# Performance work log

Measured on AMD Instinct MI355X. Metric: run time of the kernel, lower is better.

Reference implementation:

```python
import jax, jax.numpy as jnp
import numpy as np

EPS = 1e-5        # BatchNorm eps (torch default)
ALPHA = 0.2       # LeakyReLU negative slope


def _gather_nbrs(x, idx):
    # x: (B,N,C), idx: (B,P,S) -> (B,P,S,C)
    B, P, S = idx.shape
    flat = jnp.take_along_axis(x, idx.reshape(B, P * S, 1), axis=1)
    return flat.reshape(B, P, S, x.shape[-1])


def _mlp_layer(x, w, b, g, bt, m, v):
    # 1x1 Conv2d == channel matmul; BN in eval mode with running stats; ReLU.
    h = x @ w.T + b
    h = (h - m) * jax.lax.rsqrt(v + EPS) * g + bt
    return jax.nn.relu(h)


def setup_inputs() -> dict:
    key = jax.random.key(0)
    ks = jax.random.split(key, 8)
    B, N, P, S, C = 16, 4096, 1024, 32, 64
    inp = {
        "xyz": jax.random.normal(ks[0], (B, 3, N), dtype=jnp.float32),
        "points": jax.random.normal(ks[1], (B, C, N), dtype=jnp.float32),
        "fps_idx": jax.random.randint(ks[2], (B, P), 0, N, dtype=jnp.int32),
        "group_idx": jax.random.randint(ks[3], (B, P, S), 0, N, dtype=jnp.int32),
    }
    chans = [(64, 67), (64, 64), (128, 64)]
    for i, (co, ci) in enumerate(chans, start=1):
        kk = jax.random.fold_in(key, 100 + i)
        inp[f"w{i}"] = jax.random.normal(kk, (co, ci), dtype=jnp.float32) * (1.0 / np.sqrt(ci))
        inp[f"b{i}"] = jnp.zeros((co,), jnp.float32)
        inp[f"g{i}"] = jnp.ones((co,), jnp.float32)
        inp[f"beta{i}"] = jnp.zeros((co,), jnp.float32)
        inp[f"m{i}"] = jnp.zeros((co,), jnp.float32)
        inp[f"v{i}"] = jnp.ones((co,), jnp.float32)
    inp["a"] = jax.random.normal(ks[4], (3 + 128, 128), dtype=jnp.float32) * 0.1
    return inp


def reference(xyz, points, fps_idx, group_idx,
              w1, b1, g1, beta1, m1, v1,
              w2, b2, g2, beta2, m2, v2,
              w3, b3, g3, beta3, m3, v3, a):
    xyz_p = jnp.transpose(xyz, (0, 2, 1))      # (B,N,3)
    pts_p = jnp.transpose(points, (0, 2, 1))   # (B,N,C)

    # sample_and_group with precomputed fps / ball-query indices
    new_xyz = jnp.take_along_axis(xyz_p, fps_idx[:, :, None], axis=1)   # (B,P,3)
    fps_feat = jnp.take_along_axis(pts_p, fps_idx[:, :, None], axis=1)  # (B,P,C)
    grouped_xyz = _gather_nbrs(xyz_p, group_idx) - new_xyz[:, :, None, :]  # relative (B,P,S,3)
    grouped_feat = _gather_nbrs(pts_p, group_idx)                           # (B,P,S,C)

    new_points = jnp.concatenate([grouped_xyz, grouped_feat], axis=-1)  # (B,P,S,3+C)
    fps_points = jnp.concatenate([new_xyz, fps_feat], axis=-1)          # (B,P,3+C)

    layers = [(w1, b1, g1, beta1, m1, v1), (w2, b2, g2, beta2, m2, v2), (w3, b3, g3, beta3, m3, v3)]
    for (w, b, g, bt, m, v) in layers:
        new_points = _mlp_layer(new_points, w, b, g, bt, m, v)
        fps_points = _mlp_layer(fps_points, w, b, g, bt, m, v)

    # GraphAttention: delta features -> leaky-relu scores -> softmax over neighbors -> pool
    delta_p = new_xyz[:, :, None, :] - grouped_xyz        # (B,P,S,3)
    delta_h = fps_points[:, :, None, :] - new_points       # (B,P,S,D)
    e = jnp.concatenate([delta_p, delta_h], axis=-1) @ a   # (B,P,S,D)
    e = jnp.where(e > 0, e, ALPHA * e)
    attn = jax.nn.softmax(e, axis=2)                       # softmax over nsample
    pooled = jnp.sum(attn * new_points, axis=2)            # (B,P,D)

    return jnp.transpose(new_xyz, (0, 2, 1)), jnp.transpose(pooled, (0, 2, 1))
```

## Files before the change

kernel.cpp:

```cpp
#include <hip/hip_runtime.h>
#include <hip/hip_bf16.h>

#define Bn 16
#define Nn 4096
#define Pn 1024
#define Sn 32
#define Cn 64
#define EPSn 1e-5f
#define ALPHAn 0.2f

#define W1O 0
#define W2O 4352
#define W3O 8448
#define AO  16640
#define B1O 33536
#define B2O 33600
#define B3O 33664
#define WSF 33792
__device__ __align__(16) float g_W[WSF];

#define F1F 0
#define F2F 24
#define F3F 40
#define F5F 72
#define NFRAG 152
#define WFU (NFRAG * 512)
__device__ __align__(16) unsigned short g_Wf[WFU];

__device__ __align__(16) float g_pts[Bn * Nn * 68];
__device__ __align__(16) float g_fps[Bn * Pn * 132];
__device__ __align__(16) float g_tmp[Bn * Pn * 128];

typedef __attribute__((ext_vector_type(8))) short short8;
typedef __attribute__((ext_vector_type(4))) float f32x4;

__device__ __forceinline__ void split2(float v, unsigned short& hu, unsigned short& lu) {
  __hip_bfloat16 h = __float2bfloat16(v);
  float hv = __bfloat162float(h);
  __hip_bfloat16 l = __float2bfloat16(v - hv);
  hu = *(unsigned short*)&h;
  lu = *(unsigned short*)&l;
}
__device__ __forceinline__ unsigned short bfh(float v) {
  __hip_bfloat16 h = __float2bfloat16(v);
  return *(unsigned short*)&h;
}
__device__ __forceinline__ float bf2f(unsigned short u) {
  __hip_bfloat16 h = *(__hip_bfloat16*)&u;
  return __bfloat162float(h);
}

__global__ __launch_bounds__(256) void prep_kernel(
    const float* __restrict__ xyz, const float* __restrict__ points,
    const float* __restrict__ w1, const float* __restrict__ b1,
    const float* __restrict__ g1, const float* __restrict__ bt1,
    const float* __restrict__ m1, const float* __restrict__ v1,
    const float* __restrict__ w2, const float* __restrict__ b2,
    const float* __restrict__ g2, const float* __restrict__ bt2,
    const float* __restrict__ m2, const float* __restrict__ v2,
    const float* __restrict__ w3, const float* __restrict__ b3,
    const float* __restrict__ g3, const float* __restrict__ bt3,
    const float* __restrict__ m3, const float* __restrict__ v3,
    const float* __restrict__ a)
{
  if (blockIdx.x < 1024) {
    __shared__ float T[68 * 65];
    const int t = threadIdx.x;
    const int b = blockIdx.x >> 6, n0 = (blockIdx.x & 63) << 6;
    const int nn = t & 63, cgrp = t >> 6;
    #pragma unroll
    for (int k = 0; k < 16; ++k) {
      const int c = cgrp * 16 + k;
      T[c * 65 + nn] = points[(b * Cn + c) * Nn + n0 + nn];
    }
    if (cgrp == 0) {
      #pragma unroll
      for (int d = 0; d < 3; ++d)
        T[(64 + d) * 65 + nn] = xyz[(b * 3 + d) * Nn + n0 + nn];
      T[67 * 65 + nn] = 0.f;
    }
    __syncthreads();
    const int row = t >> 2, part = t & 3;
    float* dst = g_pts + (((long)b << 12) + n0 + row) * 68 + part * 16;
    #pragma unroll
    for (int j = 0; j < 4; ++j) {
      const int o = part * 16 + j * 4;
      float4 v = { T[(o + 0) * 65 + row], T[(o + 1) * 65 + row],
                   T[(o + 2) * 65 + row], T[(o + 3) * 65 + row] };
      *(float4*)(dst + j * 4) = v;
    }
    if (part == 3) {
      float4 v = { T[64 * 65 + row], T[65 * 65 + row],
                   T[66 * 65 + row], T[67 * 65 + row] };
      *(float4*)(dst + 16) = v;
    }
    return;
  }
  const int idx = (blockIdx.x - 1024) * blockDim.x + threadIdx.x;
  if (idx < WSF) {
    float val;
    if (idx < W2O) {
      const int k = idx >> 6, o = idx & 63;
      const float sc = g1[o] * rsqrtf(v1[o] + EPSn);
      val = (k < 64) ? w1[o * 67 + 3 + k] * sc
          : (k < 67) ? w1[o * 67 + (k - 64)] * sc : 0.f;
    } else if (idx < W3O) {
      const int r = idx - W2O, k = r >> 6, o = r & 63;
      val = w2[o * 64 + k] * (g2[o] * rsqrtf(v2[o] + EPSn));
    } else if (idx < AO) {
      const int r = idx - W3O, k = r >> 7, o = r & 127;
      val = w3[o * 64 + k] * (g3[o] * rsqrtf(v3[o] + EPSn));
    } else if (idx < B1O) {
      int r = idx - AO;
      const int half = r / 8448; r -= half * 8448;
      const int k = r >> 6, o = half * 64 + (r & 63);
      val = (k < 128) ? a[(3 + k) * 128 + o]
          : (k < 131) ? a[(k - 128) * 128 + o] : 0.f;
    } else if (idx < B2O) {
      const int o = idx - B1O;
      val = (b1[o] - m1[o]) * (g1[o] * rsqrtf(v1[o] + EPSn)) + bt1[o];
    } else if (idx < B3O) {
      const int o = idx - B2O;
      val = (b2[o] - m2[o]) * (g2[o] * rsqrtf(v2[o] + EPSn)) + bt2[o];
    } else {
      const int o = idx - B3O;
      val = (b3[o] - m3[o]) * (g3[o] * rsqrtf(v3[o] + EPSn)) + bt3[o];
    }
    g_W[idx] = val;
  } else if (idx < WSF + WFU) {
    const int i = idx - WSF;
    const int frag = i >> 9, r = i & 511;
    const int lane = r >> 3, j = r & 7;
    const int quad = lane >> 4, nn = lane & 15;
    int plane, n, k;
    float w;
    if (frag < F2F) {
      const int f = frag;
      plane = f & 1;
      const int c = (f >> 1) & 1, kcch = f >> 2, kc = kcch % 3, ch = kcch / 3;
      n = ch * 32 + c * 16 + nn; k = kc * 32 + quad * 8 + j;
      const float s = g1[n] * rsqrtf(v1[n] + EPSn);
      w = (k < 64) ? w1[n * 67 + 3 + k] * s
        : (k < 67) ? w1[n * 67 + (k - 64)] * s : 0.f;
    } else if (frag < F3F) {
      const int f = frag - F2F;
      plane = f & 1;
      const int c = (f >> 1) & 1, kc = (f >> 2) & 1, ch = f >> 3;
      n = ch * 32 + c * 16 + nn; k = kc * 32 + quad * 8 + j;
      w = w2[n * 64 + k] * (g2[n] * rsqrtf(v2[n] + EPSn));
    } else if (frag < F5F) {
      const int f = frag - F3F;
      plane = f & 1;
      const int c = (f >> 1) & 3, kc = (f >> 3) & 1, ch = f >> 4;
      n = ch * 64 + c * 16 + nn; k = kc * 32 + quad * 8 + j;
      w = w3[n * 64 + k] * (g3[n] * rsqrtf(v3[n] + EPSn));
    } else {
      const int f = frag - F5F;
      plane = f & 1;
      const int c = (f >> 1) & 3, kcch = f >> 3, kc = kcch % 5, ch = kcch / 5;
      n = ch * 64 + c * 16 + nn; k = kc * 32 + quad * 8 + j;
      w = (k < 128) ? a[(3 + k) * 128 + n]
        : (k < 131) ? a[(k - 128) * 128 + n] : 0.f;
    }
    unsigned short hu, lu; split2(w, hu, lu);
    g_Wf[i] = plane ? lu : hu;
  }
}

#define XAs 88
#define XHs 152

__global__ __launch_bounds__(256) void fps_kernel(
    const int* __restrict__ fps_idx, float* __restrict__ out)
{
  __shared__ __align__(16) unsigned char LB[30736];
  unsigned short* XAh = (unsigned short*)(LB + 0);
  unsigned short* XAl = (unsigned short*)(LB + 5632);
  unsigned short* XHh = (unsigned short*)(LB + 11264);
  unsigned short* XHl = (unsigned short*)(LB + 20992);
  unsigned short* ZS  = (unsigned short*)(LB + 30720);

  const int t = threadIdx.x, lane = t & 63, w = t >> 6;
  const int quad = lane >> 4, nn = lane & 15;
  const int ch = w >> 1, cl = w & 1;
  const int blk = ((blockIdx.x & 7) << 6) | (blockIdx.x >> 3);
  const int g0 = blk * 32;

  if (t < 4) ((float*)ZS)[t] = 0.f;

  {
    const int s0 = t >> 3, cg = t & 7;
    const int gp = g0 + s0, b = gp >> 10, p = gp & 1023;
    const int fi = fps_idx[gp];
    const float* frow = g_pts + (((long)b << 12) + fi) * 68;
    const int c0 = cg * 8;
    const float4 va = *(const float4*)(frow + c0);
    const float4 vb = *(const float4*)(frow + c0 + 4);
    short8 hv, lv;
    unsigned short hu, lu;
    split2(va.x, hu, lu); hv[0] = (short)hu; lv[0] = (short)lu;
    split2(va.y, hu, lu); hv[1] = (short)hu; lv[1] = (short)lu;
    split2(va.z, hu, lu); hv[2] = (short)hu; lv[2] = (short)lu;
    split2(va.w, hu, lu); hv[3] = (short)hu; lv[3] = (short)lu;
    split2(vb.x, hu, lu); hv[4] = (short)hu; lv[4] = (short)lu;
    split2(vb.y, hu, lu); hv[5] = (short)hu; lv[5] = (short)lu;
    split2(vb.z, hu, lu); hv[6] = (short)hu; lv[6] = (short)lu;
    split2(vb.w, hu, lu); hv[7] = (short)hu; lv[7] = (short)lu;
    *(short8*)(XAh + s0 * XAs + c0) = hv;
    *(short8*)(XAl + s0 * XAs + c0) = lv;
    if (cg == 0) {
      #pragma unroll
      for (int d = 0; d < 3; ++d) {
        const float v = frow[64 + d];
        unsigned short h2, l2; split2(v, h2, l2);
        XAh[s0 * XAs + 64 + d] = h2; XAl[s0 * XAs + 64 + d] = l2;
        XHh[s0 * XHs + 128 + d] = h2; XHl[s0 * XHs + 128 + d] = l2;
        out[(b * 3 + d) * Pn + p] = v;
        g_fps[(long)gp * 132 + 128 + d] = v;
      }
    } else if (cg == 1) {
      #pragma unroll
      for (int j = 0; j < 13; ++j) { XAh[s0 * XAs + 67 + j] = 0; XAl[s0 * XAs + 67 + j] = 0; }
    } else if (cg == 2) {
      #pragma unroll
      for (int j = 0; j < 13; ++j) { XHh[s0 * XHs + 131 + j] = 0; XHl[s0 * XHs + 131 + j] = 0; }
    }
  }
  __syncthreads();

#define MFMA_BF16 __builtin_amdgcn_mfma_f32_16x16x32_bf16
#define TERM3(Ci, Ahh, All, Bh, Bl) \
    Ci = MFMA_BF16(Ahh, Bh, Ci, 0, 0, 0); \
    Ci = MFMA_BF16(Ahh, Bl, Ci, 0, 0, 0); \
    Ci = MFMA_BF16(All, Bh, Ci, 0, 0, 0);

  f32x4 C[4];
  const int col1 = w * 16 + nn;

  C[0] = (f32x4){0.f,0.f,0.f,0.f}; C[1] = C[0];
  #pragma unroll
  for (int kc = 0; kc < 3; ++kc) {
    const int ka = kc * 32 + quad * 8;
    const short8 A0h = (ka < 80) ? *(const short8*)(XAh + nn * XAs + ka) : *(const short8*)ZS;
    const short8 A0l = (ka < 80) ? *(const short8*)(XAl + nn * XAs + ka) : *(const short8*)ZS;
    const short8 A1h = (ka < 80) ? *(const short8*)(XAh + (16 + nn) * XAs + ka) : *(const short8*)ZS;
    const short8 A1l = (ka < 80) ? *(const short8*)(XAl + (16 + nn) * XAs + ka) : *(const short8*)ZS;
    const unsigned short* pf = g_Wf + (((ch * 3 + kc) * 2 + cl) * 2) * 512 + lane * 8;
    const short8 Bh = *(const short8*)pf, Bl = *(const short8*)(pf + 512);
    TERM3(C[0], A0h, A0l, Bh, Bl);
    TERM3(C[1], A1h, A1l, Bh, Bl);
  }
  #pragma unroll
  for (int mi = 0; mi < 2; ++mi)
    #pragma unroll
    for (int r = 0; r < 4; ++r) {
      const float v = fmaxf(C[mi][r] + g_W[B1O + col1], 0.f);
      unsigned short hu, lu; split2(v, hu, lu);
      XHh[(mi * 16 + quad * 4 + r) * XHs + col1] = hu;
      XHl[(mi * 16 + quad * 4 + r) * XHs + col1] = lu;
    }
  __syncthreads();

  C[0] = (f32x4){0.f,0.f,0.f,0.f}; C[1] = C[0];
  #pragma unroll
  for (int kc = 0; kc < 2; ++kc) {
    const int ka = kc * 32 + quad * 8;
    const short8 A0h = *(const short8*)(XHh + nn * XHs + ka);
    const short8 A0l = *(const short8*)(XHl + nn * XHs + ka);
    const short8 A1h = *(const short8*)(XHh + (16 + nn) * XHs + ka);
    const short8 A1l = *(const short8*)(XHl + (16 + nn) * XHs + ka);
    const unsigned short* pf = g_Wf + (F2F + ((ch * 2 + kc) * 2 + cl) * 2) * 512 + lane * 8;
    const short8 Bh = *(const short8*)pf, Bl = *(const short8*)(pf + 512);
    TERM3(C[0], A0h, A0l, Bh, Bl);
    TERM3(C[1], A1h, A1l, Bh, Bl);
  }
  __syncthreads();
  #pragma unroll
  for (int mi = 0; mi < 2; ++mi)
    #pragma unroll
    for (int r = 0; r < 4; ++r) {
      const float v = fmaxf(C[mi][r] + g_W[B2O + col1], 0.f);
      unsigned short hu, lu; split2(v, hu, lu);
      XAh[(mi * 16 + quad * 4 + r) * XAs + col1] = hu;
      XAl[(mi * 16 + quad * 4 + r) * XAs + col1] = lu;
    }
  __syncthreads();

  #pragma unroll
  for (int i = 0; i < 4; ++i) C[i] = (f32x4){0.f,0.f,0.f,0.f};
  #pragma unroll
  for (int kc = 0; kc < 2; ++kc) {
    const int ka = kc * 32 + quad * 8;
    const short8 A0h = *(const short8*)(XAh + nn * XAs + ka);
    const short8 A0l = *(const short8*)(XAl + nn * XAs + ka);
    const short8 A1h = *(const short8*)(XAh + (16 + nn) * XAs + ka);
    const short8 A1l = *(const short8*)(XAl + (16 + nn) * XAs + ka);
    #pragma unroll
    for (int c2 = 0; c2 < 2; ++c2) {
      const unsigned short* pf = g_Wf + (F3F + ((ch * 2 + kc) * 4 + cl * 2 + c2) * 2) * 512 + lane * 8;
      const short8 Bh = *(const short8*)pf, Bl = *(const short8*)(pf + 512);
      TERM3(C[0 + c2], A0h, A0l, Bh, Bl);
      TERM3(C[2 + c2], A1h, A1l, Bh, Bl);
    }
  }
  __syncthreads();
  #pragma unroll
  for (int c2 = 0; c2 < 2; ++c2) {
    const int col = w * 32 + c2 * 16 + nn;
    #pragma unroll
    for (int mi = 0; mi < 2; ++mi)
      #pragma unroll
      for (int r = 0; r < 4; ++r) {
        const float v = fmaxf(C[mi * 2 + c2][r] + g_W[B3O + col], 0.f);
        unsigned short hu, lu; split2(v, hu, lu);
        XHh[(mi * 16 + quad * 4 + r) * XHs + col] = hu;
        XHl[(mi * 16 + quad * 4 + r) * XHs + col] = lu;
      }
  }
  __syncthreads();

  #pragma unroll
  for (int i = 0; i < 4; ++i) C[i] = (f32x4){0.f,0.f,0.f,0.f};
  #pragma unroll
  for (int kc = 0; kc < 5; ++kc) {
    const int ka = kc * 32 + quad * 8;
    const short8 A0h = (ka < 144) ? *(const short8*)(XHh + nn * XHs + ka) : *(const short8*)ZS;
    const short8 A0l = (ka < 144) ? *(const short8*)(XHl + nn * XHs + ka) : *(const short8*)ZS;
    const short8 A1h = (ka < 144) ? *(const short8*)(XHh + (16 + nn) * XHs + ka) : *(const short8*)ZS;
    const short8 A1l = (ka < 144) ? *(const short8*)(XHl + (16 + nn) * XHs + ka) : *(const short8*)ZS;
    #pragma unroll
    for (int c2 = 0; c2 < 2; ++c2) {
      const unsigned short* pf = g_Wf + (F5F + ((ch * 5 + kc) * 4 + cl * 2 + c2) * 2) * 512 + lane * 8;
      const short8 Bh = *(const short8*)pf, Bl = *(const short8*)(pf + 512);
      TERM3(C[0 + c2], A0h, A0l, Bh, Bl);
      TERM3(C[2 + c2], A1h, A1l, Bh, Bl);
    }
  }
  #pragma unroll
  for (int c2 = 0; c2 < 2; ++c2) {
    const int col = w * 32 + c2 * 16 + nn;
    #pragma unroll
    for (int mi = 0; mi < 2; ++mi)
      #pragma unroll
      for (int r = 0; r < 4; ++r)
        g_fps[(long)(g0 + mi * 16 + quad * 4 + r) * 132 + col] = C[mi * 2 + c2][r];
  }
}

__global__ __launch_bounds__(256) void transpose_out(float* __restrict__ out)
{
  __shared__ float T[64 * 129];
  const int t = threadIdx.x;
  const int b = blockIdx.x >> 4, p0 = (blockIdx.x & 15) << 6;
  const int c = t & 127, ph = t >> 7;
  #pragma unroll
  for (int pp = 0; pp < 32; ++pp) {
    const int pi = ph * 32 + pp;
    T[pi * 129 + c] = g_tmp[(((long)b << 10) + p0 + pi) * 128 + c];
  }
  __syncthreads();
  const int pn = t & 63, cg = t >> 6;
  #pragma unroll
  for (int k = 0; k < 32; ++k) {
    const int cc = cg * 32 + k;
    out[Bn * 3 * Pn + ((b << 7) + cc) * Pn + p0 + pn] = T[pn * 129 + cc];
  }
}

#define OXA 0
#define OXH 5632
#define OFS 15360
#define OZS 15872
#define LDSB 15888

__global__ __launch_bounds__(256, 8) void fused_kernel(
    const int* __restrict__ group_idx)
{
  __shared__ __align__(16) unsigned char LB[LDSB];
  unsigned short* XAh = (unsigned short*)(LB + OXA);
  unsigned short* XHh = (unsigned short*)(LB + OXH);
  float*          FS  = (float*)(LB + OFS);
  unsigned short* ZS  = (unsigned short*)(LB + OZS);

  const int t = threadIdx.x, lane = t & 63, w = t >> 6;
  const int quad = lane >> 4, nn = lane & 15;
  const int ch = w >> 1, cl = w & 1;
  const int g = ((blockIdx.x & 7) << 11) | (blockIdx.x >> 3);
  const int b = g >> 10;

  if (t < 128) FS[t] = g_fps[(long)g * 132 + t];
  if (t < 4) ((float*)ZS)[t] = 0.f;

  {
    const int s0 = t >> 3, cg = t & 7;
    const int gi = group_idx[g * Sn + s0];
    const float* prow = g_pts + (((long)b << 12) + gi) * 68;
    const int c0 = cg * 8;
    const float4 va = *(const float4*)(prow + c0);
    const float4 vb = *(const float4*)(prow + c0 + 4);
    short8 hv;
    hv[0] = (short)bfh(va.x); hv[1] = (short)bfh(va.y);
    hv[2] = (short)bfh(va.z); hv[3] = (short)bfh(va.w);
    hv[4] = (short)bfh(vb.x); hv[5] = (short)bfh(vb.y);
    hv[6] = (short)bfh(vb.z); hv[7] = (short)bfh(vb.w);
    *(short8*)(XAh + s0 * XAs + c0) = hv;
    if (cg == 0) {
      #pragma unroll
      for (int d = 0; d < 3; ++d) {
        const float r = prow[64 + d] - g_fps[(long)g * 132 + 128 + d];
        const unsigned short hu = bfh(r);
        XAh[s0 * XAs + 64 + d] = hu;
        XHh[s0 * XHs + 128 + d] = hu;
      }
    } else if (cg == 1) {
      #pragma unroll
      for (int j = 0; j < 13; ++j) XAh[s0 * XAs + 67 + j] = 0;
    } else if (cg == 2) {
      #pragma unroll
      for (int j = 0; j < 13; ++j) XHh[s0 * XHs + 131 + j] = 0;
    }
  }
  __syncthreads();

  f32x4 C[4];
  const int col1 = w * 16 + nn;

  C[0] = (f32x4){0.f,0.f,0.f,0.f}; C[1] = C[0];
  #pragma unroll
  for (int kc = 0; kc < 3; ++kc) {
    const int ka = kc * 32 + quad * 8;
    const short8 A0 = (ka < 80) ? *(const short8*)(XAh + nn * XAs + ka) : *(const short8*)ZS;
    const short8 A1 = (ka < 80) ? *(const short8*)(XAh + (16 + nn) * XAs + ka) : *(const short8*)ZS;
    const unsigned short* pf = g_Wf + (((ch * 3 + kc) * 2 + cl) * 2) * 512 + lane * 8;
    const short8 Bh = *(const short8*)pf, Bl = *(const short8*)(pf + 512);
    C[0] = MFMA_BF16(A0, Bh, C[0], 0, 0, 0);
    C[0] = MFMA_BF16(A0, Bl, C[0], 0, 0, 0);
    C[1] = MFMA_BF16(A1, Bh, C[1], 0, 0, 0);
    C[1] = MFMA_BF16(A1, Bl, C[1], 0, 0, 0);
  }
  #pragma unroll
  for (int mi = 0; mi < 2; ++mi)
    #pragma unroll
    for (int r = 0; r < 4; ++r)
      XHh[(mi * 16 + quad * 4 + r) * XHs + col1] =
          bfh(fmaxf(C[mi][r] + g_W[B1O + col1], 0.f));
  __syncthreads();

  C[0] = (f32x4){0.f,0.f,0.f,0.f}; C[1] = C[0];
  #pragma unroll
  for (int kc = 0; kc < 2; ++kc) {
    const int ka = kc * 32 + quad * 8;
    const short8 A0 = *(const short8*)(XHh + nn * XHs + ka);
    const short8 A1 = *(const short8*)(XHh + (16 + nn) * XHs + ka);
    const unsigned short* pf = g_Wf + (F2F + ((ch * 2 + kc) * 2 + cl) * 2) * 512 + lane * 8;
    const short8 Bh = *(const short8*)pf, Bl = *(const short8*)(pf + 512);
    C[0] = MFMA_BF16(A0, Bh, C[0], 0, 0, 0);
    C[0] = MFMA_BF16(A0, Bl, C[0], 0, 0, 0);
    C[1] = MFMA_BF16(A1, Bh, C[1], 0, 0, 0);
    C[1] = MFMA_BF16(A1, Bl, C[1], 0, 0, 0);
  }
  #pragma unroll
  for (int mi = 0; mi < 2; ++mi)
    #pragma unroll
    for (int r = 0; r < 4; ++r)
      XAh[(mi * 16 + quad * 4 + r) * XAs + col1] =
          bfh(fmaxf(C[mi][r] + g_W[B2O + col1], 0.f));
  __syncthreads();

  #pragma unroll
  for (int i = 0; i < 4; ++i) C[i] = (f32x4){0.f,0.f,0.f,0.f};
  #pragma unroll
  for (int kc = 0; kc < 2; ++kc) {
    const int ka = kc * 32 + quad * 8;
    const short8 A0 = *(const short8*)(XAh + nn * XAs + ka);
    const short8 A1 = *(const short8*)(XAh + (16 + nn) * XAs + ka);
    #pragma unroll
    for (int c2 = 0; c2 < 2; ++c2) {
      const unsigned short* pf = g_Wf + (F3F + ((ch * 2 + kc) * 4 + cl * 2 + c2) * 2) * 512 + lane * 8;
      const short8 Bh = *(const short8*)pf, Bl = *(const short8*)(pf + 512);
      C[0 + c2] = MFMA_BF16(A0, Bh, C[0 + c2], 0, 0, 0);
      C[0 + c2] = MFMA_BF16(A0, Bl, C[0 + c2], 0, 0, 0);
      C[2 + c2] = MFMA_BF16(A1, Bh, C[2 + c2], 0, 0, 0);
      C[2 + c2] = MFMA_BF16(A1, Bl, C[2 + c2], 0, 0, 0);
    }
  }
  #pragma unroll
  for (int c2 = 0; c2 < 2; ++c2) {
    const int col = w * 32 + c2 * 16 + nn;
    #pragma unroll
    for (int mi = 0; mi < 2; ++mi)
      #pragma unroll
      for (int r = 0; r < 4; ++r)
        XHh[(mi * 16 + quad * 4 + r) * XHs + col] =
            bfh(fmaxf(C[mi * 2 + c2][r] + g_W[B3O + col], 0.f));
  }
  __syncthreads();

  #pragma unroll
  for (int i = 0; i < 4; ++i) C[i] = (f32x4){0.f,0.f,0.f,0.f};
  #pragma unroll
  for (int kc = 0; kc < 5; ++kc) {
    const int ka = kc * 32 + quad * 8;
    const short8 A0 = (ka < 144) ? *(const short8*)(XHh + nn * XHs + ka) : *(const short8*)ZS;
    const short8 A1 = (ka < 144) ? *(const short8*)(XHh + (16 + nn) * XHs + ka) : *(const short8*)ZS;
    #pragma unroll
    for (int c2 = 0; c2 < 2; ++c2) {
      const unsigned short* pf = g_Wf + (F5F + ((ch * 5 + kc) * 4 + cl * 2 + c2) * 2) * 512 + lane * 8;
      const short8 Bh = *(const short8*)pf, Bl = *(const short8*)(pf + 512);
      C[0 + c2] = MFMA_BF16(A0, Bh, C[0 + c2], 0, 0, 0);
      C[0 + c2] = MFMA_BF16(A0, Bl, C[0 + c2], 0, 0, 0);
      C[2 + c2] = MFMA_BF16(A1, Bh, C[2 + c2], 0, 0, 0);
      C[2 + c2] = MFMA_BF16(A1, Bl, C[2 + c2], 0, 0, 0);
    }
  }

  #pragma unroll
  for (int c2 = 0; c2 < 2; ++c2) {
    const int col = w * 32 + c2 * 16 + nn;
    const float eb = FS[col];
    float m_ = -3.4e38f;
    #pragma unroll
    for (int mi = 0; mi < 2; ++mi)
      #pragma unroll
      for (int r = 0; r < 4; ++r) {
        float e = eb - C[mi * 2 + c2][r];
        e = (e > 0.f) ? e : ALPHAn * e;
        C[mi * 2 + c2][r] = e;
        m_ = fmaxf(m_, e);
      }
    m_ = fmaxf(m_, __shfl_xor(m_, 16));
    m_ = fmaxf(m_, __shfl_xor(m_, 32));
    float den = 0.f, pool = 0.f;
    #pragma unroll
    for (int mi = 0; mi < 2; ++mi)
      #pragma unroll
      for (int r = 0; r < 4; ++r) {
        const float wgt = __expf(C[mi * 2 + c2][r] - m_);
        den += wgt;
        pool = fmaf(wgt, bf2f(XHh[(mi * 16 + quad * 4 + r) * XHs + col]), pool);
      }
    den  += __shfl_xor(den, 16);  den  += __shfl_xor(den, 32);
    pool += __shfl_xor(pool, 16); pool += __shfl_xor(pool, 32);
    if (quad == 0) g_tmp[(long)g * 128 + col] = pool / den;
  }
}

extern "C" void kernel_launch(void* const* d_in, const int* in_sizes, int n_in,
                              void* d_out, int out_size, void* d_ws, size_t ws_size,
                              hipStream_t stream) {
  const float* xyz       = (const float*)d_in[0];
  const float* points    = (const float*)d_in[1];
  const int*   fps_idx   = (const int*)d_in[2];
  const int*   group_idx = (const int*)d_in[3];

  const int prep_blocks = 1024 + (WSF + WFU + 255) / 256;
  prep_kernel<<<prep_blocks, 256, 0, stream>>>(
      xyz, points,
      (const float*)d_in[4],  (const float*)d_in[5],
      (const float*)d_in[6],  (const float*)d_in[7],
      (const float*)d_in[8],  (const float*)d_in[9],
      (const float*)d_in[10], (const float*)d_in[11],
      (const float*)d_in[12], (const float*)d_in[13],
      (const float*)d_in[14], (const float*)d_in[15],
      (const float*)d_in[16], (const float*)d_in[17],
      (const float*)d_in[18], (const float*)d_in[19],
      (const float*)d_in[20], (const float*)d_in[21],
      (const float*)d_in[22]);

  fps_kernel<<<512, 256, 0, stream>>>(fps_idx, (float*)d_out);

  fused_kernel<<<Bn * Pn, 256, 0, stream>>>(group_idx);

  transpose_out<<<Bn * 16, 256, 0, stream>>>((float*)d_out);
}
```

Before: 238.8 us.

## Fold biases into accumulators, pack bf16 stores, use exp2 softmax, split fps blocks

The MLP biases and the negated fps feature now initialise the MFMA accumulators, which removes the separate bias adds and the FS shared staging buffer. LOG2E is folded into the attention weights so the softmax can use a native exp2. Bf16 stores use packed cvt instructions paired across lanes via shuffle, and the pooling reads fp32 activations kept in registers instead of bf16 values reloaded from LDS. The division becomes an rcp. The fps kernel processes 16 points per block over twice as many blocks, with less LDS per block. Pooling now uses unrounded activations and the rcp is approximate, so results differ slightly.

```diff
diff --git a/kernel.cpp b/kernel.cpp
--- a/kernel.cpp
+++ b/kernel.cpp
@@ -8,6 +8,7 @@
 #define Cn 64
 #define EPSn 1e-5f
 #define ALPHAn 0.2f
+#define LOG2E 1.44269504088896341f
 
 #define W1O 0
 #define W2O 4352
@@ -45,10 +46,19 @@
   __hip_bfloat16 h = __float2bfloat16(v);
   return *(unsigned short*)&h;
 }
-__device__ __forceinline__ float bf2f(unsigned short u) {
-  __hip_bfloat16 h = *(__hip_bfloat16*)&u;
-  return __bfloat162float(h);
-}
+
+#define MFMA_BF16 __builtin_amdgcn_mfma_f32_16x16x32_bf16
+#define TERM3(Ci, Ahh, All, Bh, Bl) \
+    Ci = MFMA_BF16(Ahh, Bh, Ci, 0, 0, 0); \
+    Ci = MFMA_BF16(Ahh, Bl, Ci, 0, 0, 0); \
+    Ci = MFMA_BF16(All, Bh, Ci, 0, 0, 0);
+
+#define ST_PK(BUF, ST, ROW, COLE, V) do {                                   \
+    float _pp = __shfl_xor((V), 1);                                         \
+    unsigned _pk;                                                           \
+    asm("v_cvt_pk_bf16_f32 %0, %1, %2" : "=v"(_pk) : "v"(V), "v"(_pp));     \
+    if (!(nn & 1)) *(unsigned*)((BUF) + (ROW) * (ST) + (COLE)) = _pk;       \
+  } while (0)
 
 __global__ __launch_bounds__(256) void prep_kernel(
     const float* __restrict__ xyz, const float* __restrict__ points,
@@ -159,8 +169,8 @@
       plane = f & 1;
       const int c = (f >> 1) & 3, kcch = f >> 3, kc = kcch % 5, ch = kcch / 5;
       n = ch * 64 + c * 16 + nn; k = kc * 32 + quad * 8 + j;
-      w = (k < 128) ? a[(3 + k) * 128 + n]
-        : (k < 131) ? a[(k - 128) * 128 + n] : 0.f;
+      w = ((k < 128) ? a[(3 + k) * 128 + n]
+        : (k < 131) ? a[(k - 128) * 128 + n] : 0.f) * LOG2E;
     }
     unsigned short hu, lu; split2(w, hu, lu);
     g_Wf[i] = plane ? lu : hu;
@@ -173,22 +183,22 @@
 __global__ __launch_bounds__(256) void fps_kernel(
     const int* __restrict__ fps_idx, float* __restrict__ out)
 {
-  __shared__ __align__(16) unsigned char LB[30736];
+  __shared__ __align__(16) unsigned char LB[15376];
   unsigned short* XAh = (unsigned short*)(LB + 0);
-  unsigned short* XAl = (unsigned short*)(LB + 5632);
-  unsigned short* XHh = (unsigned short*)(LB + 11264);
-  unsigned short* XHl = (unsigned short*)(LB + 20992);
-  unsigned short* ZS  = (unsigned short*)(LB + 30720);
+  unsigned short* XAl = (unsigned short*)(LB + 2816);
+  unsigned short* XHh = (unsigned short*)(LB + 5632);
+  unsigned short* XHl = (unsigned short*)(LB + 10496);
+  unsigned short* ZS  = (unsigned short*)(LB + 15360);
 
   const int t = threadIdx.x, lane = t & 63, w = t >> 6;
   const int quad = lane >> 4, nn = lane & 15;
   const int ch = w >> 1, cl = w & 1;
-  const int blk = ((blockIdx.x & 7) << 6) | (blockIdx.x >> 3);
-  const int g0 = blk * 32;
+  const int blk = ((blockIdx.x & 7) << 7) | (blockIdx.x >> 3);
+  const int g0 = blk * 16;
 
   if (t < 4) ((float*)ZS)[t] = 0.f;
 
-  {
+  if (t < 128) {
     const int s0 = t >> 3, cg = t & 7;
     const int gp = g0 + s0, b = gp >> 10, p = gp & 1023;
     const int fi = fps_idx[gp];
@@ -214,7 +224,8 @@
         const float v = frow[64 + d];
         unsigned short h2, l2; split2(v, h2, l2);
         XAh[s0 * XAs + 64 + d] = h2; XAl[s0 * XAs + 64 + d] = l2;
-        XHh[s0 * XHs + 128 + d] = h2; XHl[s0 * XHs + 128 + d] = l2;
+        XHh[s0 * XHs + 128 + d] = h2; XHl[s0 * XHs + 131 - 3 + d] = l2;
+        XHl[s0 * XHs + 128 + d] = l2;
         out[(b * 3 + d) * Pn + p] = v;
         g_fps[(long)gp * 132 + 128 + d] = v;
       }
@@ -228,79 +239,70 @@
   }
   __syncthreads();
 
-#define MFMA_BF16 __builtin_amdgcn_mfma_f32_16x16x32_bf16
-#define TERM3(Ci, Ahh, All, Bh, Bl) \
-    Ci = MFMA_BF16(Ahh, Bh, Ci, 0, 0, 0); \
-    Ci = MFMA_BF16(Ahh, Bl, Ci, 0, 0, 0); \
-    Ci = MFMA_BF16(All, Bh, Ci, 0, 0, 0);
-
-  f32x4 C[4];
+  f32x4 C[2];
   const int col1 = w * 16 + nn;
 
-  C[0] = (f32x4){0.f,0.f,0.f,0.f}; C[1] = C[0];
+  {
+    const float bb = g_W[B1O + col1];
+    C[0] = (f32x4){bb, bb, bb, bb};
+  }
   #pragma unroll
   for (int kc = 0; kc < 3; ++kc) {
     const int ka = kc * 32 + quad * 8;
     const short8 A0h = (ka < 80) ? *(const short8*)(XAh + nn * XAs + ka) : *(const short8*)ZS;
     const short8 A0l = (ka < 80) ? *(const short8*)(XAl + nn * XAs + ka) : *(const short8*)ZS;
-    const short8 A1h = (ka < 80) ? *(const short8*)(XAh + (16 + nn) * XAs + ka) : *(const short8*)ZS;
-    const short8 A1l = (ka < 80) ? *(const short8*)(XAl + (16 + nn) * XAs + ka) : *(const short8*)ZS;
     const unsigned short* pf = g_Wf + (((ch * 3 + kc) * 2 + cl) * 2) * 512 + lane * 8;
     const short8 Bh = *(const short8*)pf, Bl = *(const short8*)(pf + 512);
     TERM3(C[0], A0h, A0l, Bh, Bl);
-    TERM3(C[1], A1h, A1l, Bh, Bl);
-  }
-  #pragma unroll
-  for (int mi = 0; mi < 2; ++mi)
-    #pragma unroll
-    for (int r = 0; r < 4; ++r) {
-      const float v = fmaxf(C[mi][r] + g_W[B1O + col1], 0.f);
-      unsigned short hu, lu; split2(v, hu, lu);
-      XHh[(mi * 16 + quad * 4 + r) * XHs + col1] = hu;
-      XHl[(mi * 16 + quad * 4 + r) * XHs + col1] = lu;
-    }
-  __syncthreads();
-
-  C[0] = (f32x4){0.f,0.f,0.f,0.f}; C[1] = C[0];
+  }
+  #pragma unroll
+  for (int r = 0; r < 4; ++r) {
+    const float v = fmaxf(C[0][r], 0.f);
+    unsigned short hu, lu; split2(v, hu, lu);
+    XHh[(quad * 4 + r) * XHs + col1] = hu;
+    XHl[(quad * 4 + r) * XHs + col1] = lu;
+  }
+  __syncthreads();
+
+  {
+    const float bb = g_W[B2O + col1];
+    C[0] = (f32x4){bb, bb, bb, bb};
+  }
   #pragma unroll
   for (int kc = 0; kc < 2; ++kc) {
     const int ka = kc * 32 + quad * 8;
     const short8 A0h = *(const short8*)(XHh + nn * XHs + ka);
     const short8 A0l = *(const short8*)(XHl + nn * XHs + ka);
-    const short8 A1h = *(const short8*)(XHh + (16 + nn) * XHs + ka);
-    const short8 A1l = *(const short8*)(XHl + (16 + nn) * XHs + ka);
     const unsigned short* pf = g_Wf + (F2F + ((ch * 2 + kc) * 2 + cl) * 2) * 512 + lane * 8;
     const short8 Bh = *(const short8*)pf, Bl = *(const short8*)(pf + 512);
     TERM3(C[0], A0h, A0l, Bh, Bl);
-    TERM3(C[1], A1h, A1l, Bh, Bl);
-  }
-  __syncthreads();
-  #pragma unroll
-  for (int mi = 0; mi < 2; ++mi)
-    #pragma unroll
-    for (int r = 0; r < 4; ++r) {
-      const float v = fmaxf(C[mi][r] + g_W[B2O + col1], 0.f);
-      unsigned short hu, lu; split2(v, hu, lu);
-      XAh[(mi * 16 + quad * 4 + r) * XAs + col1] = hu;
-      XAl[(mi * 16 + quad * 4 + r) * XAs + col1] = lu;
-    }
-  __syncthreads();
-
-  #pragma unroll
-  for (int i = 0; i < 4; ++i) C[i] = (f32x4){0.f,0.f,0.f,0.f};
+  }
+  __syncthreads();
+  #pragma unroll
+  for (int r = 0; r < 4; ++r) {
+    const float v = fmaxf(C[0][r], 0.f);
+    unsigned short hu, lu; split2(v, hu, lu);
+    XAh[(quad * 4 + r) * XAs + col1] = hu;
+    XAl[(quad * 4 + r) * XAs + col1] = lu;
+  }
+  __syncthreads();
+
+  {
+    const float b0 = g_W[B3O + w * 32 + nn];
+    const float b1 = g_W[B3O + w * 32 + 16 + nn];
+    C[0] = (f32x4){b0, b0, b0, b0};
+    C[1] = (f32x4){b1, b1, b1, b1};
+  }
   #pragma unroll
   for (int kc = 0; kc < 2; ++kc) {
     const int ka = kc * 32 + quad * 8;
     const short8 A0h = *(const short8*)(XAh + nn * XAs + ka);
     const short8 A0l = *(const short8*)(XAl + nn * XAs + ka);
-    const short8 A1h = *(const short8*)(XAh + (16 + nn) * XAs + ka);
-    const short8 A1l = *(const short8*)(XAl + (16 + nn) * XAs + ka);
     #pragma unroll
     for (int c2 = 0; c2 < 2; ++c2) {
       const unsigned short* pf = g_Wf + (F3F + ((ch * 2 + kc) * 4 + cl * 2 + c2) * 2) * 512 + lane * 8;
       const short8 Bh = *(const short8*)pf, Bl = *(const short8*)(pf + 512);
-      TERM3(C[0 + c2], A0h, A0l, Bh, Bl);
-      TERM3(C[2 + c2], A1h, A1l, Bh, Bl);
+      TERM3(C[c2], A0h, A0l, Bh, Bl);
     }
   }
   __syncthreads();
@@ -308,42 +310,34 @@
   for (int c2 = 0; c2 < 2; ++c2) {
     const int col = w * 32 + c2 * 16 + nn;
     #pragma unroll
-    for (int mi = 0; mi < 2; ++mi)
-      #pragma unroll
-      for (int r = 0; r < 4; ++r) {
-        const float v = fmaxf(C[mi * 2 + c2][r] + g_W[B3O + col], 0.f);
-        unsigned short hu, lu; split2(v, hu, lu);
-        XHh[(mi * 16 + quad * 4 + r) * XHs + col] = hu;
-        XHl[(mi * 16 + quad * 4 + r) * XHs + col] = lu;
-      }
-  }
-  __syncthreads();
-
-  #pragma unroll
-  for (int i = 0; i < 4; ++i) C[i] = (f32x4){0.f,0.f,0.f,0.f};
+    for (int r = 0; r < 4; ++r) {
+      const float v = fmaxf(C[c2][r], 0.f);
+      unsigned short hu, lu; split2(v, hu, lu);
+      XHh[(quad * 4 + r) * XHs + col] = hu;
+      XHl[(quad * 4 + r) * XHs + col] = lu;
+    }
+  }
+  __syncthreads();
+
+  C[0] = (f32x4){0.f,0.f,0.f,0.f}; C[1] = C[0];
   #pragma unroll
   for (int kc = 0; kc < 5; ++kc) {
     const int ka = kc * 32 + quad * 8;
     const short8 A0h = (ka < 144) ? *(const short8*)(XHh + nn * XHs + ka) : *(const short8*)ZS;
     const short8 A0l = (ka < 144) ? *(const short8*)(XHl + nn * XHs + ka) : *(const short8*)ZS;
-    const short8 A1h = (ka < 144) ? *(const short8*)(XHh + (16 + nn) * XHs + ka) : *(const short8*)ZS;
-    const short8 A1l = (ka < 144) ? *(const short8*)(XHl + (16 + nn) * XHs + ka) : *(const short8*)ZS;
     #pragma unroll
     for (int c2 = 0; c2 < 2; ++c2) {
       const unsigned short* pf = g_Wf + (F5F + ((ch * 5 + kc) * 4 + cl * 2 + c2) * 2) * 512 + lane * 8;
       const short8 Bh = *(const short8*)pf, Bl = *(const short8*)(pf + 512);
-      TERM3(C[0 + c2], A0h, A0l, Bh, Bl);
-      TERM3(C[2 + c2], A1h, A1l, Bh, Bl);
+      TERM3(C[c2], A0h, A0l, Bh, Bl);
     }
   }
   #pragma unroll
   for (int c2 = 0; c2 < 2; ++c2) {
     const int col = w * 32 + c2 * 16 + nn;
     #pragma unroll
-    for (int mi = 0; mi < 2; ++mi)
-      #pragma unroll
-      for (int r = 0; r < 4; ++r)
-        g_fps[(long)(g0 + mi * 16 + quad * 4 + r) * 132 + col] = C[mi * 2 + c2][r];
+    for (int r = 0; r < 4; ++r)
+      g_fps[(long)(g0 + quad * 4 + r) * 132 + col] = C[c2][r];
   }
 }
 
@@ -369,9 +363,8 @@
 
 #define OXA 0
 #define OXH 5632
-#define OFS 15360
-#define OZS 15872
-#define LDSB 15888
+#define OZS 15360
+#define LDSB 15376
 
 __global__ __launch_bounds__(256, 8) void fused_kernel(
     const int* __restrict__ group_idx)
@@ -379,7 +372,6 @@
   __shared__ __align__(16) unsigned char LB[LDSB];
   unsigned short* XAh = (unsigned short*)(LB + OXA);
   unsigned short* XHh = (unsigned short*)(LB + OXH);
-  float*          FS  = (float*)(LB + OFS);
   unsigned short* ZS  = (unsigned short*)(LB + OZS);
 
   const int t = threadIdx.x, lane = t & 63, w = t >> 6;
@@ -388,7 +380,6 @@
   const int g = ((blockIdx.x & 7) << 11) | (blockIdx.x >> 3);
   const int b = g >> 10;
 
-  if (t < 128) FS[t] = g_fps[(long)g * 132 + t];
   if (t < 4) ((float*)ZS)[t] = 0.f;
 
   {
@@ -398,12 +389,13 @@
     const int c0 = cg * 8;
     const float4 va = *(const float4*)(prow + c0);
     const float4 vb = *(const float4*)(prow + c0 + 4);
-    short8 hv;
-    hv[0] = (short)bfh(va.x); hv[1] = (short)bfh(va.y);
-    hv[2] = (short)bfh(va.z); hv[3] = (short)bfh(va.w);
-    hv[4] = (short)bfh(vb.x); hv[5] = (short)bfh(vb.y);
-    hv[6] = (short)bfh(vb.z); hv[7] = (short)bfh(vb.w);
-    *(short8*)(XAh + s0 * XAs + c0) = hv;
+    unsigned p0, p1, p2, p3;
+    asm("v_cvt_pk_bf16_f32 %0, %1, %2" : "=v"(p0) : "v"(va.x), "v"(va.y));
+    asm("v_cvt_pk_bf16_f32 %0, %1, %2" : "=v"(p1) : "v"(va.z), "v"(va.w));
+    asm("v_cvt_pk_bf16_f32 %0, %1, %2" : "=v"(p2) : "v"(vb.x), "v"(vb.y));
+    asm("v_cvt_pk_bf16_f32 %0, %1, %2" : "=v"(p3) : "v"(vb.z), "v"(vb.w));
+    uint4 hv = {p0, p1, p2, p3};
+    *(uint4*)(XAh + s0 * XAs + c0) = hv;
     if (cg == 0) {
       #pragma unroll
       for (int d = 0; d < 3; ++d) {
@@ -424,8 +416,13 @@
 
   f32x4 C[4];
   const int col1 = w * 16 + nn;
-
-  C[0] = (f32x4){0.f,0.f,0.f,0.f}; C[1] = C[0];
+  const int colE1 = w * 16 + (nn & ~1);
+
+  {
+    const float bb = g_W[B1O + col1];
+    C[0] = (f32x4){bb, bb, bb, bb};
+    C[1] = C[0];
+  }
   #pragma unroll
   for (int kc = 0; kc < 3; ++kc) {
     const int ka = kc * 32 + quad * 8;
@@ -441,12 +438,17 @@
   #pragma unroll
   for (int mi = 0; mi < 2; ++mi)
     #pragma unroll
-    for (int r = 0; r < 4; ++r)
-      XHh[(mi * 16 + quad * 4 + r) * XHs + col1] =
-          bfh(fmaxf(C[mi][r] + g_W[B1O + col1], 0.f));
-  __syncthreads();
-
-  C[0] = (f32x4){0.f,0.f,0.f,0.f}; C[1] = C[0];
+    for (int r = 0; r < 4; ++r) {
+      const float v = fmaxf(C[mi][r], 0.f);
+      ST_PK(XHh, XHs, mi * 16 + quad * 4 + r, colE1, v);
+    }
+  __syncthreads();
+
+  {
+    const float bb = g_W[B2O + col1];
+    C[0] = (f32x4){bb, bb, bb, bb};
+    C[1] = C[0];
+  }
   #pragma unroll
   for (int kc = 0; kc < 2; ++kc) {
     const int ka = kc * 32 + quad * 8;
@@ -462,13 +464,20 @@
   #pragma unroll
   for (int mi = 0; mi < 2; ++mi)
     #pragma unroll
-    for (int r = 0; r < 4; ++r)
-      XAh[(mi * 16 + quad * 4 + r) * XAs + col1] =
-          bfh(fmaxf(C[mi][r] + g_W[B2O + col1], 0.f));
-  __syncthreads();
-
-  #pragma unroll
-  for (int i = 0; i < 4; ++i) C[i] = (f32x4){0.f,0.f,0.f,0.f};
+    for (int r = 0; r < 4; ++r) {
+      const float v = fmaxf(C[mi][r], 0.f);
+      ST_PK(XAh, XAs, mi * 16 + quad * 4 + r, colE1, v);
+    }
+  __syncthreads();
+
+  {
+    const float b0 = g_W[B3O + w * 32 + nn];
+    const float b1 = g_W[B3O + w * 32 + 16 + nn];
+    C[0] = (f32x4){b0, b0, b0, b0};
+    C[1] = (f32x4){b1, b1, b1, b1};
+    C[2] = C[0];
+    C[3] = C[1];
+  }
   #pragma unroll
   for (int kc = 0; kc < 2; ++kc) {
     const int ka = kc * 32 + quad * 8;
@@ -484,20 +493,30 @@
       C[2 + c2] = MFMA_BF16(A1, Bl, C[2 + c2], 0, 0, 0);
     }
   }
+  f32x4 H[4];
   #pragma unroll
   for (int c2 = 0; c2 < 2; ++c2) {
-    const int col = w * 32 + c2 * 16 + nn;
+    const int colE = w * 32 + c2 * 16 + (nn & ~1);
     #pragma unroll
     for (int mi = 0; mi < 2; ++mi)
       #pragma unroll
-      for (int r = 0; r < 4; ++r)
-        XHh[(mi * 16 + quad * 4 + r) * XHs + col] =
-            bfh(fmaxf(C[mi * 2 + c2][r] + g_W[B3O + col], 0.f));
-  }
-  __syncthreads();
-
-  #pragma unroll
-  for (int i = 0; i < 4; ++i) C[i] = (f32x4){0.f,0.f,0.f,0.f};
+      for (int r = 0; r < 4; ++r) {
+        const int idx = mi * 2 + c2;
+        const float v = fmaxf(C[idx][r], 0.f);
+        H[idx][r] = v;
+        ST_PK(XHh, XHs, mi * 16 + quad * 4 + r, colE, v);
+      }
+  }
+  __syncthreads();
+
+  {
+    const float e0 = g_fps[(long)g * 132 + w * 32 + nn];
+    const float e1 = g_fps[(long)g * 132 + w * 32 + 16 + nn];
+    C[0] = (f32x4){-e0, -e0, -e0, -e0};
+    C[1] = (f32x4){-e1, -e1, -e1, -e1};
+    C[2] = C[0];
+    C[3] = C[1];
+  }
   #pragma unroll
   for (int kc = 0; kc < 5; ++kc) {
     const int ka = kc * 32 + quad * 8;
@@ -516,32 +535,35 @@
 
   #pragma unroll
   for (int c2 = 0; c2 < 2; ++c2) {
-    const int col = w * 32 + c2 * 16 + nn;
-    const float eb = FS[col];
-    float m_ = -3.4e38f;
+    float tmin = 3.4e38f;
     #pragma unroll
     for (int mi = 0; mi < 2; ++mi)
       #pragma unroll
       for (int r = 0; r < 4; ++r) {
-        float e = eb - C[mi * 2 + c2][r];
-        e = (e > 0.f) ? e : ALPHAn * e;
-        C[mi * 2 + c2][r] = e;
-        m_ = fmaxf(m_, e);
+        const int idx = mi * 2 + c2;
+        const float cv = C[idx][r];
+        const float tv = fminf(cv, 0.2f * cv);
+        C[idx][r] = tv;
+        tmin = fminf(tmin, tv);
       }
-    m_ = fmaxf(m_, __shfl_xor(m_, 16));
-    m_ = fmaxf(m_, __shfl_xor(m_, 32));
+    tmin = fminf(tmin, __shfl_xor(tmin, 16));
+    tmin = fminf(tmin, __shfl_xor(tmin, 32));
     float den = 0.f, pool = 0.f;
     #pragma unroll
     for (int mi = 0; mi < 2; ++mi)
       #pragma unroll
       for (int r = 0; r < 4; ++r) {
-        const float wgt = __expf(C[mi * 2 + c2][r] - m_);
+        const int idx = mi * 2 + c2;
+        const float wgt = __builtin_amdgcn_exp2f(tmin - C[idx][r]);
         den += wgt;
-        pool = fmaf(wgt, bf2f(XHh[(mi * 16 + quad * 4 + r) * XHs + col]), pool);
+        pool = fmaf(wgt, H[idx][r], pool);
       }
     den  += __shfl_xor(den, 16);  den  += __shfl_xor(den, 32);
     pool += __shfl_xor(pool, 16); pool += __shfl_xor(pool, 32);
-    if (quad == 0) g_tmp[(long)g * 128 + col] = pool / den;
+    if (quad == 0) {
+      const int col = w * 32 + c2 * 16 + nn;
+      g_tmp[(long)g * 128 + col] = pool * __builtin_amdgcn_rcpf(den);
+    }
   }
 }
 
@@ -567,7 +589,7 @@
       (const float*)d_in[20], (const float*)d_in[21],
       (const float*)d_in[22]);
 
-  fps_kernel<<<512, 256, 0, stream>>>(fps_idx, (float*)d_out);
+  fps_kernel<<<1024, 256, 0, stream>>>(fps_idx, (float*)d_out);
 
   fused_kernel<<<Bn * Pn, 256, 0, stream>>>(group_idx);
 
```

New measurement: 250.5 us. 1.05x slower.
